# Optimization experiments

Measured on AMD Instinct MI355X. Metric: run time of the kernel, lower is better.

The kernel has to match this reference:

```python
import jax, jax.numpy as jnp
import numpy as np

B, V, J = 1024, 6890, 24
P_FEAT = (J - 1) * 9  # 207 pose-blendshape features
SMPL_PARENTS = [-1, 0, 0, 0, 1, 2, 3, 4, 5, 6, 7, 8, 9, 9, 9, 12, 13, 14, 16, 17, 18, 19, 20, 21]


def setup_inputs() -> dict:
    key = jax.random.key(0)
    ks = jax.random.split(key, 7)
    return {
        "betas": jax.random.normal(ks[0], (B, 10), jnp.float32),
        "full_pose": jax.random.normal(ks[1], (B, 72), jnp.float32) * 0.3,
        "v_template": jax.random.normal(ks[2], (1, V, 3), jnp.float32),
        "shapedirs": jax.random.normal(ks[3], (V, 3, 10), jnp.float32) * 0.01,
        "posedirs": jax.random.normal(ks[4], (P_FEAT, V * 3), jnp.float32) * 0.01,
        "J_regressor": jax.nn.softmax(jax.random.normal(ks[5], (J, V), jnp.float32), axis=-1),
        "lbs_weights": jax.nn.softmax(jax.random.normal(ks[6], (V, J), jnp.float32) * 4.0, axis=-1),
        "parents": jnp.array(SMPL_PARENTS, dtype=jnp.int32),
    }


def batch_rodrigues(rot_vecs):
    # rot_vecs: [..., 3] axis-angle -> [..., 3, 3] rotation matrices
    angle = jnp.linalg.norm(rot_vecs + 1e-8, axis=-1, keepdims=True)  # [...,1]
    axis = rot_vecs / angle
    s = jnp.sin(angle)[..., None]
    c = jnp.cos(angle)[..., None]
    kx, ky, kz = axis[..., 0], axis[..., 1], axis[..., 2]
    zeros = jnp.zeros_like(kx)
    K = jnp.stack([zeros, -kz, ky, kz, zeros, -kx, -ky, kx, zeros], axis=-1)
    K = K.reshape(rot_vecs.shape[:-1] + (3, 3))
    eye = jnp.eye(3, dtype=rot_vecs.dtype)
    return eye + s * K + (1.0 - c) * (K @ K)


def reference(betas, full_pose, v_template, shapedirs, posedirs, J_regressor, lbs_weights, parents):
    p = [int(x) for x in np.asarray(jax.device_get(parents))]  # static kinematic tree
    b = betas.shape[0]

    # 1) shape blendshapes: minimal shape
    v_shaped = v_template + jnp.einsum("bl,vkl->bvk", betas, shapedirs)  # [B,V,3]

    # 2) rest joints
    J_rest = jnp.einsum("jv,bvk->bjk", J_regressor, v_shaped)  # [B,J,3]

    # 3) pose rotations + pose blendshapes
    rot_mats = batch_rodrigues(full_pose.reshape(b, J, 3))  # [B,J,3,3]
    eye = jnp.eye(3, dtype=rot_mats.dtype)
    pose_feature = (rot_mats[:, 1:] - eye).reshape(b, P_FEAT)  # [B,207]
    v_posed = v_shaped + (pose_feature @ posedirs).reshape(b, V, 3)

    # 4) kinematic chain (sequential composition over fixed 24 joints)
    rel_joints = J_rest.at[:, 1:].add(-J_rest[:, np.array(p[1:])])  # [B,J,3]
    Tm = jnp.zeros((b, J, 4, 4), dtype=rot_mats.dtype)
    Tm = Tm.at[:, :, :3, :3].set(rot_mats)
    Tm = Tm.at[:, :, :3, 3].set(rel_joints)
    Tm = Tm.at[:, :, 3, 3].set(1.0)
    chain = [Tm[:, 0]]
    for i in range(1, J):
        chain.append(chain[p[i]] @ Tm[:, i])
    transforms = jnp.stack(chain, axis=1)  # [B,J,4,4]

    J_posed = transforms[:, :, :3, 3]  # [B,J,3]

    # relative bone transforms: subtract rotated rest joints from translation
    RJ = jnp.einsum("bjmn,bjn->bjm", transforms[:, :, :3, :3], J_rest)
    A = transforms.at[:, :, :3, 3].add(-RJ)  # [B,J,4,4]

    # 5) linear blend skinning: per-vertex weighted transform then apply
    T = jnp.einsum("vj,bjmn->bvmn", lbs_weights, A)  # [B,V,4,4]
    verts = jnp.einsum("bvmn,bvn->bvm", T[:, :, :3, :3], v_posed) + T[:, :, :3, 3]

    return verts, J_posed, J_rest, A, v_shaped
```

## Files before the change

kernel.cpp:

```cpp
#include <hip/hip_runtime.h>
#include <hip/hip_bf16.h>

#define BDIM 1024
#define VDIM 6890
#define NJ   24
#define NCOL (VDIM*3)
#define KPAD 224
#define NPAD 20736
#define NB   8
#define VPAD 6912

#define OUT_VERTS   0
#define OUT_JPOSED  21166080
#define OUT_JREST   21239808
#define OUT_A       21313536
#define OUT_VSHAPED 21706752

#define SCRF_PDT    0
#define SCRF_PF     2322432
#define SCRF_JTJS   2437120

#define WSB_PDT   0u
#define WSB_PF    9289728u
#define WSB_JTJS  9748480u
#define WSB_WHI   9752064u
#define WSB_WLO   10194432u
#define WS_NEED   10636800u

typedef __hip_bfloat16 bf16;
typedef unsigned short ushort_t;
typedef __attribute__((ext_vector_type(8))) short  short8;
typedef __attribute__((ext_vector_type(4))) float  float4v;

__device__ __forceinline__ bf16  tob(float x) { return __float2bfloat16(x); }

__device__ __forceinline__ ushort_t bf16_rne(float x) {
    unsigned u = __builtin_bit_cast(unsigned, x);
    unsigned r = (u + 0x7FFFu + ((u >> 16) & 1u)) >> 16;
    return (ushort_t)r;
}
__device__ __forceinline__ float bf16_to_f(ushort_t h) {
    unsigned u = ((unsigned)h) << 16;
    return __builtin_bit_cast(float, u);
}

__global__ __launch_bounds__(256) void k_jtjs(const float* __restrict__ jreg,
        const float* __restrict__ vt, const float* __restrict__ sd,
        float* __restrict__ jtjs) {
    int j = blockIdx.x;
    int tid = threadIdx.x;
    float acc[33];
#pragma unroll
    for (int i = 0; i < 33; i++) acc[i] = 0.f;
    for (int v = tid; v < VDIM; v += 256) {
        float r = jreg[j*VDIM + v];
#pragma unroll
        for (int m = 0; m < 3; m++) {
            acc[m] += r * vt[v*3+m];
#pragma unroll
            for (int l = 0; l < 10; l++)
                acc[3 + m*10 + l] += r * sd[(v*3+m)*10 + l];
        }
    }
    __shared__ float red[4][33];
    int lane = tid & 63, wid = tid >> 6;
#pragma unroll
    for (int i = 0; i < 33; i++) {
        float x = acc[i];
        for (int off = 32; off > 0; off >>= 1) x += __shfl_down(x, off);
        if (lane == 0) red[wid][i] = x;
    }
    __syncthreads();
    if (tid < 33)
        jtjs[j*33 + tid] = red[0][tid] + red[1][tid] + red[2][tid] + red[3][tid];
}

__global__ __launch_bounds__(256) void k_transpose(const float* __restrict__ pd,
        bf16* __restrict__ pdt) {
    __shared__ bf16 tile[32][65];
    int nt = blockIdx.x * 64;
    int kt = blockIdx.y * 32;
    int t = threadIdx.x;
    for (int i = t; i < 32*64; i += 256) {
        int kk = i >> 6, nn = i & 63;
        int k = kt + kk, n = nt + nn;
        float v = 0.f;
        if (k < 207 && n < NCOL) v = pd[k*NCOL + n];
        tile[kk][nn] = tob(v);
    }
    __syncthreads();
    for (int i = t; i < 32*64; i += 256) {
        int kk = i & 31, nn = i >> 5;
        pdt[(nt + nn)*KPAD + kt + kk] = tile[kk][nn];
    }
}

__global__ __launch_bounds__(256) void k_wpack(const float* __restrict__ lbs,
        ushort_t* __restrict__ whi, ushort_t* __restrict__ wlo) {
    int idx = blockIdx.x*256 + threadIdx.x;
    if (idx >= VPAD*32) return;
    int v = idx >> 5, j = idx & 31;
    float x = (v < VDIM && j < 24) ? lbs[v*24 + j] : 0.f;
    ushort_t h = bf16_rne(x);
    whi[idx] = h;
    wlo[idx] = bf16_rne(x - bf16_to_f(h));
}

__global__ __launch_bounds__(64) void k_pose(const float* __restrict__ betas,
        const float* __restrict__ pose, const int* __restrict__ parents,
        const float* __restrict__ jtjs, float* __restrict__ out,
        bf16* __restrict__ wspf) {
    int b = blockIdx.x, t = threadIdx.x;
    __shared__ float R[24][9];
    __shared__ float jrest[24][3];
    __shared__ float rel[24][3];
    __shared__ float ch[24][12];
    __shared__ int par[24];
    if (t < 24) {
        par[t] = parents[t];
        float rx = pose[b*72 + t*3 + 0];
        float ry = pose[b*72 + t*3 + 1];
        float rz = pose[b*72 + t*3 + 2];
        float ax = rx + 1e-8f, ay = ry + 1e-8f, az = rz + 1e-8f;
        float angle = sqrtf(ax*ax + ay*ay + az*az);
        float inv = 1.0f / angle;
        float kx = rx*inv, ky = ry*inv, kz = rz*inv;
        float s = sinf(angle), c = cosf(angle);
        float t1 = 1.0f - c;
        float q = kx*kx + ky*ky + kz*kz;
        R[t][0] = 1.f + t1*(kx*kx - q);
        R[t][1] = -s*kz + t1*kx*ky;
        R[t][2] =  s*ky + t1*kx*kz;
        R[t][3] =  s*kz + t1*kx*ky;
        R[t][4] = 1.f + t1*(ky*ky - q);
        R[t][5] = -s*kx + t1*ky*kz;
        R[t][6] = -s*ky + t1*kx*kz;
        R[t][7] =  s*kx + t1*ky*kz;
        R[t][8] = 1.f + t1*(kz*kz - q);
    }
    __syncthreads();
    for (int i = t; i < KPAD; i += 64) {
        float pf = 0.f;
        if (i < 207) {
            int j = i/9 + 1, e = i - (j-1)*9;
            pf = R[j][e] - ((e == 0 || e == 4 || e == 8) ? 1.f : 0.f);
        }
        wspf[b*KPAD + i] = tob(pf);
    }
    for (int i = t; i < 72; i += 64) {
        int j = i/3, k = i - j*3;
        const float* JJ = &jtjs[j*33];
        float s = JJ[k];
#pragma unroll
        for (int l = 0; l < 10; l++) s += JJ[3 + k*10 + l] * betas[b*10 + l];
        jrest[j][k] = s;
        out[OUT_JREST + b*72 + i] = s;
    }
    __syncthreads();
    for (int i = t; i < 72; i += 64) {
        int j = i/3, k = i - j*3;
        rel[j][k] = jrest[j][k] - (j > 0 ? jrest[par[j]][k] : 0.f);
    }
    __syncthreads();
    if (t < 12) {
        int m = t >> 2, n = t & 3;
        ch[0][t] = (n < 3) ? R[0][m*3+n] : rel[0][m];
    }
    __syncthreads();
    for (int i = 1; i < 24; i++) {
        float val = 0.f;
        if (t < 12) {
            int m = t >> 2, n = t & 3;
            int p = par[i];
            if (n < 3)
                val = ch[p][m*4+0]*R[i][n] + ch[p][m*4+1]*R[i][3+n] + ch[p][m*4+2]*R[i][6+n];
            else
                val = ch[p][m*4+0]*rel[i][0] + ch[p][m*4+1]*rel[i][1]
                    + ch[p][m*4+2]*rel[i][2] + ch[p][m*4+3];
        }
        if (t < 12) ch[i][t] = val;
        __syncthreads();
    }
    for (int i = t; i < 72; i += 64) {
        int j = i/3, k = i - j*3;
        out[OUT_JPOSED + b*72 + i] = ch[j][k*4+3];
    }
    for (int i = t; i < 384; i += 64) {
        int j = i >> 4, e = i & 15, m = e >> 2, n = e & 3;
        float v;
        if (m < 3) {
            if (n < 3) v = ch[j][m*4+n];
            else v = ch[j][m*4+3] - (ch[j][m*4+0]*jrest[j][0] + ch[j][m*4+1]*jrest[j][1]
                                   + ch[j][m*4+2]*jrest[j][2]);
        } else v = (n == 3) ? 1.f : 0.f;
        out[OUT_A + b*384 + i] = v;
    }
}

__global__ __launch_bounds__(256) void k_gemmlbs(const bf16* __restrict__ wspf,
        const bf16* __restrict__ wspdt, const float* __restrict__ betas,
        const float* __restrict__ sd, const float* __restrict__ vt,
        const ushort_t* __restrict__ whi, const ushort_t* __restrict__ wlo,
        const float* __restrict__ Amat, float* __restrict__ out) {
    __shared__ float dtile[32][196];
    const ushort_t* pf  = (const ushort_t*)wspf;
    const ushort_t* pdt = (const ushort_t*)wspdt;
    int tid  = threadIdx.x;
    int lane = tid & 63, wave = tid >> 6;
    int l15 = lane & 15, quad = lane >> 4;
    int m0 = blockIdx.y * 32;
    int v0 = blockIdx.x * 64;
    int cb = wave * 48;
    int colb = v0*3 + cb;

    {
        float4v acc[2][3] = {};
        for (int c = 0; c < 7; c++) {
            short8 a[2], bb[3];
#pragma unroll
            for (int mf = 0; mf < 2; mf++)
                a[mf] = *reinterpret_cast<const short8*>(pf + (m0 + mf*16 + l15)*KPAD + c*32 + quad*8);
#pragma unroll
            for (int nf = 0; nf < 3; nf++)
                bb[nf] = *reinterpret_cast<const short8*>(pdt + (colb + nf*16 + l15)*KPAD + c*32 + quad*8);
#pragma unroll
            for (int mf = 0; mf < 2; mf++)
#pragma unroll
                for (int nf = 0; nf < 3; nf++)
                    acc[mf][nf] = __builtin_amdgcn_mfma_f32_16x16x32_bf16(a[mf], bb[nf], acc[mf][nf], 0, 0, 0);
        }
#pragma unroll
        for (int mf = 0; mf < 2; mf++)
#pragma unroll
            for (int nf = 0; nf < 3; nf++)
#pragma unroll
                for (int r = 0; r < 4; r++)
                    dtile[mf*16 + quad*4 + r][cb + nf*16 + l15] = acc[mf][nf][r];
    }
    __syncthreads();

    int wv = __builtin_amdgcn_readfirstlane(wave);
    int v = v0 + lane;
    float* vsh = out + OUT_VSHAPED;
    if (v < VDIM) {
        float vtv[3];
#pragma unroll
        for (int m = 0; m < 3; m++) vtv[m] = vt[v*3 + m];
        float sdv[30];
#pragma unroll
        for (int i = 0; i < 30; i++) sdv[i] = sd[v*30 + i];
#pragma unroll 1
        for (int bb2 = 0; bb2 < 8; bb2++) {
            int b  = m0 + wv*8 + bb2;
            int bl = wv*8 + bb2;
            float vs[3];
#pragma unroll
            for (int m = 0; m < 3; m++) {
                float s = vtv[m];
#pragma unroll
                for (int l = 0; l < 10; l++) s += betas[b*10 + l] * sdv[m*10 + l];
                vs[m] = s;
            }
            int base = b*NCOL + v*3;
#pragma unroll
            for (int n = 0; n < 3; n++) {
                float d = dtile[bl][lane*3 + n];
                dtile[bl][lane*3 + n] = vs[n] + d;
                vsh[base + n] = vs[n];
            }
        }
    }
    __syncthreads();

    short8 bhi[4], blo[4];
#pragma unroll
    for (int nf = 0; nf < 4; nf++) {
        int vv = v0 + nf*16 + l15;
        bhi[nf] = *reinterpret_cast<const short8*>(whi + vv*32 + quad*8);
        blo[nf] = *reinterpret_cast<const short8*>(wlo + vv*32 + quad*8);
    }
    bool aval = (quad < 3) && (l15 < 12);
#pragma unroll 1
    for (int bb2 = 0; bb2 < 8; bb2++) {
        int b  = m0 + wv*8 + bb2;
        int bl = wv*8 + bb2;
        float af[8];
#pragma unroll
        for (int i = 0; i < 8; i++)
            af[i] = aval ? Amat[(size_t)b*384 + (quad*8 + i)*16 + l15] : 0.f;
        short8 ahi, alo;
#pragma unroll
        for (int i = 0; i < 8; i++) {
            ushort_t h = bf16_rne(af[i]);
            ahi[i] = (short)h;
            alo[i] = (short)bf16_rne(af[i] - bf16_to_f(h));
        }
#pragma unroll
        for (int nf = 0; nf < 4; nf++) {
            float4v acc = {};
            acc = __builtin_amdgcn_mfma_f32_16x16x32_bf16(ahi, bhi[nf], acc, 0, 0, 0);
            acc = __builtin_amdgcn_mfma_f32_16x16x32_bf16(alo, bhi[nf], acc, 0, 0, 0);
            acc = __builtin_amdgcn_mfma_f32_16x16x32_bf16(ahi, blo[nf], acc, 0, 0, 0);
            int vl = nf*16 + l15;
            float vp0 = dtile[bl][vl*3 + 0];
            float vp1 = dtile[bl][vl*3 + 1];
            float vp2 = dtile[bl][vl*3 + 2];
            if (quad < 3 && v0 + vl < VDIM) {
                float o = acc[3] + acc[0]*vp0 + acc[1]*vp1 + acc[2]*vp2;
                out[(size_t)b*NCOL + (v0 + vl)*3 + quad] = o;
            }
        }
    }
}

__global__ __launch_bounds__(256) void k_posegemm(const bf16* __restrict__ wspf,
        const bf16* __restrict__ wspdt, float* __restrict__ dout) {
    const ushort_t* pf  = (const ushort_t*)wspf;
    const ushort_t* pdt = (const ushort_t*)wspdt;
    int lane = threadIdx.x & 63;
    int wave = threadIdx.x >> 6;
    int l15 = lane & 15, quad = lane >> 4;
    int m0 = blockIdx.y * 32;
    int n0 = blockIdx.x * 256 + wave * 64;
    float4v acc[2][4] = {};
    for (int c = 0; c < 7; c++) {
        short8 a[2], bb[4];
#pragma unroll
        for (int mf = 0; mf < 2; mf++)
            a[mf] = *reinterpret_cast<const short8*>(pf + (m0 + mf*16 + l15)*KPAD + c*32 + quad*8);
#pragma unroll
        for (int nf = 0; nf < 4; nf++)
            bb[nf] = *reinterpret_cast<const short8*>(pdt + (n0 + nf*16 + l15)*KPAD + c*32 + quad*8);
#pragma unroll
        for (int mf = 0; mf < 2; mf++)
#pragma unroll
            for (int nf = 0; nf < 4; nf++)
                acc[mf][nf] = __builtin_amdgcn_mfma_f32_16x16x32_bf16(a[mf], bb[nf], acc[mf][nf], 0, 0, 0);
    }
#pragma unroll
    for (int mf = 0; mf < 2; mf++)
#pragma unroll
        for (int nf = 0; nf < 4; nf++) {
            int col = n0 + nf*16 + l15;
            if (col < NCOL) {
#pragma unroll
                for (int r = 0; r < 4; r++) {
                    int row = m0 + mf*16 + quad*4 + r;
                    dout[row*NCOL + col] = acc[mf][nf][r];
                }
            }
        }
}

__global__ __launch_bounds__(256) void k_lbs(const float* __restrict__ betas,
        const float* __restrict__ sd, const float* __restrict__ vt,
        const float* __restrict__ lbs, const float* __restrict__ Amat,
        float* __restrict__ out) {
    int tid = threadIdx.x;
    int v = blockIdx.x*256 + tid;
    if (v >= VDIM) return;
    int b0 = blockIdx.y * NB;
    float w[24];
    {
        const float4v* W4 = reinterpret_cast<const float4v*>(lbs + v*24);
#pragma unroll
        for (int q = 0; q < 6; q++) {
            float4v x = W4[q];
#pragma unroll
            for (int e = 0; e < 4; e++) w[q*4+e] = x[e];
        }
    }
    float vtv[3];
#pragma unroll
    for (int m = 0; m < 3; m++) vtv[m] = vt[v*3 + m];
    float sdv[30];
#pragma unroll
    for (int i = 0; i < 30; i++) sdv[i] = sd[v*30 + i];
    float* vsh = out + OUT_VSHAPED;
#pragma unroll 1
    for (int bb = 0; bb < NB; bb++) {
        int b = b0 + bb;
        const float* __restrict__ Ab = Amat + (size_t)b*384;
        float T[12];
#pragma unroll
        for (int e = 0; e < 12; e++) T[e] = 0.f;
#pragma unroll
        for (int j = 0; j < 24; j++) {
#pragma unroll
            for (int e = 0; e < 12; e++)
                T[e] = fmaf(w[j], Ab[j*16 + e], T[e]);
        }
        float vs[3];
#pragma unroll
        for (int m = 0; m < 3; m++) {
            float s = vtv[m];
#pragma unroll
            for (int l = 0; l < 10; l++) s += betas[b*10 + l] * sdv[m*10 + l];
            vs[m] = s;
        }
        int base = b*NCOL + v*3;
        float vp0 = vs[0] + vsh[base + 0];
        float vp1 = vs[1] + vsh[base + 1];
        float vp2 = vs[2] + vsh[base + 2];
#pragma unroll
        for (int m = 0; m < 3; m++) {
            float o = T[m*4+3] + T[m*4]*vp0 + T[m*4+1]*vp1 + T[m*4+2]*vp2;
            out[base + m] = o;
            vsh[base + m] = vs[m];
        }
    }
}

extern "C" void kernel_launch(void* const* d_in, const int* in_sizes, int n_in,
                              void* d_out, int out_size, void* d_ws, size_t ws_size,
                              hipStream_t stream) {
    const float *betas = nullptr, *pose = nullptr, *vt = nullptr, *sd = nullptr,
                *pd = nullptr, *jreg = nullptr, *lbs = nullptr;
    const int* parents = nullptr;
    for (int i = 0; i < n_in; i++) {
        switch (in_sizes[i]) {
            case 10240:   betas = (const float*)d_in[i]; break;
            case 73728:   pose  = (const float*)d_in[i]; break;
            case 20670:   vt    = (const float*)d_in[i]; break;
            case 206700:  sd    = (const float*)d_in[i]; break;
            case 4278690: pd    = (const float*)d_in[i]; break;
            case 24:      parents = (const int*)d_in[i]; break;
            case 165360:
                if (!jreg) jreg = (const float*)d_in[i];
                else       lbs  = (const float*)d_in[i];
                break;
            default: break;
        }
    }
    float* out = (float*)d_out;
    if (d_ws && ws_size >= (size_t)WS_NEED) {
        bf16*     ws_pdt  = (bf16*)((char*)d_ws + WSB_PDT);
        bf16*     ws_pf   = (bf16*)((char*)d_ws + WSB_PF);
        float*    ws_jtjs = (float*)((char*)d_ws + WSB_JTJS);
        ushort_t* ws_whi  = (ushort_t*)((char*)d_ws + WSB_WHI);
        ushort_t* ws_wlo  = (ushort_t*)((char*)d_ws + WSB_WLO);
        k_jtjs<<<24, 256, 0, stream>>>(jreg, vt, sd, ws_jtjs);
        k_transpose<<<dim3(324, 7), 256, 0, stream>>>(pd, ws_pdt);
        k_wpack<<<(VPAD*32 + 255)/256, 256, 0, stream>>>(lbs, ws_whi, ws_wlo);
        k_pose<<<BDIM, 64, 0, stream>>>(betas, pose, parents, ws_jtjs, out, ws_pf);
        k_gemmlbs<<<dim3(108, 32), 256, 0, stream>>>(ws_pf, ws_pdt, betas, sd, vt,
                                                     ws_whi, ws_wlo, out + OUT_A, out);
    } else {
        bf16*  ws_pdt  = (bf16*)(out + SCRF_PDT);
        bf16*  ws_pf   = (bf16*)(out + SCRF_PF);
        float* ws_jtjs = out + SCRF_JTJS;
        k_jtjs<<<24, 256, 0, stream>>>(jreg, vt, sd, ws_jtjs);
        k_transpose<<<dim3(324, 7), 256, 0, stream>>>(pd, ws_pdt);
        k_pose<<<BDIM, 64, 0, stream>>>(betas, pose, parents, ws_jtjs, out, ws_pf);
        k_posegemm<<<dim3(81, 32), 256, 0, stream>>>(ws_pf, ws_pdt, out + OUT_VSHAPED);
        k_lbs<<<dim3(27, BDIM/NB), 256, 0, stream>>>(betas, sd, vt, lbs, out + OUT_A, out);
    }
}
```

Baseline: 300.2 us.

## Precompute bf16 hi/lo A matrices, pad vertex tile to float4, merge prep kernels

Merges the lbs-weight packing into the joint-regressor prep kernel, removing one launch. k_pose now also writes the bone transforms as bf16 hi/lo split matrices, so the LBS stage loads ready MFMA operands instead of loading and converting fp32 per batch. The posed-vertex shared tile is stored with a 4-float stride, which allows vectorized float4 reads and writes. A __syncthreads between phases is dropped, on the reasoning that each wave only touches its own rows. The cost is extra workspace and global traffic for the A hi/lo buffers, and a larger shared-memory tile.

```diff
diff --git a/kernel.cpp b/kernel.cpp
--- a/kernel.cpp
+++ b/kernel.cpp
@@ -25,7 +25,9 @@
 #define WSB_JTJS  9748480u
 #define WSB_WHI   9752064u
 #define WSB_WLO   10194432u
-#define WS_NEED   10636800u
+#define WSB_AHI   10636800u
+#define WSB_ALO   11685376u
+#define WS_NEED   12733952u
 
 typedef __hip_bfloat16 bf16;
 typedef unsigned short ushort_t;
@@ -44,9 +46,21 @@
     return __builtin_bit_cast(float, u);
 }
 
-__global__ __launch_bounds__(256) void k_jtjs(const float* __restrict__ jreg,
+__global__ __launch_bounds__(256) void k_prep(const float* __restrict__ jreg,
         const float* __restrict__ vt, const float* __restrict__ sd,
-        float* __restrict__ jtjs) {
+        const float* __restrict__ lbs, float* __restrict__ jtjs,
+        ushort_t* __restrict__ whi, ushort_t* __restrict__ wlo) {
+    if (blockIdx.x >= 24) {
+        if (!whi) return;
+        int idx = (blockIdx.x - 24)*256 + threadIdx.x;
+        if (idx >= VPAD*32) return;
+        int v = idx >> 5, j = idx & 31;
+        float x = (v < VDIM && j < 24) ? lbs[v*24 + j] : 0.f;
+        ushort_t h = bf16_rne(x);
+        whi[idx] = h;
+        wlo[idx] = bf16_rne(x - bf16_to_f(h));
+        return;
+    }
     int j = blockIdx.x;
     int tid = threadIdx.x;
     float acc[33];
@@ -95,21 +109,11 @@
     }
 }
 
-__global__ __launch_bounds__(256) void k_wpack(const float* __restrict__ lbs,
-        ushort_t* __restrict__ whi, ushort_t* __restrict__ wlo) {
-    int idx = blockIdx.x*256 + threadIdx.x;
-    if (idx >= VPAD*32) return;
-    int v = idx >> 5, j = idx & 31;
-    float x = (v < VDIM && j < 24) ? lbs[v*24 + j] : 0.f;
-    ushort_t h = bf16_rne(x);
-    whi[idx] = h;
-    wlo[idx] = bf16_rne(x - bf16_to_f(h));
-}
-
 __global__ __launch_bounds__(64) void k_pose(const float* __restrict__ betas,
         const float* __restrict__ pose, const int* __restrict__ parents,
         const float* __restrict__ jtjs, float* __restrict__ out,
-        bf16* __restrict__ wspf) {
+        bf16* __restrict__ wspf, ushort_t* __restrict__ ahi,
+        ushort_t* __restrict__ alo) {
     int b = blockIdx.x, t = threadIdx.x;
     __shared__ float R[24][9];
     __shared__ float jrest[24][3];
@@ -195,14 +199,30 @@
         } else v = (n == 3) ? 1.f : 0.f;
         out[OUT_A + b*384 + i] = v;
     }
+    if (ahi) {
+        for (int i = t; i < 512; i += 64) {
+            int e = i >> 5, j = i & 31;
+            float v = 0.f;
+            if (j < 24 && e < 12) {
+                int m = e >> 2, n = e & 3;
+                if (n < 3) v = ch[j][m*4+n];
+                else v = ch[j][m*4+3] - (ch[j][m*4+0]*jrest[j][0] + ch[j][m*4+1]*jrest[j][1]
+                                       + ch[j][m*4+2]*jrest[j][2]);
+            }
+            ushort_t h = bf16_rne(v);
+            ahi[b*512 + i] = h;
+            alo[b*512 + i] = bf16_rne(v - bf16_to_f(h));
+        }
+    }
 }
 
 __global__ __launch_bounds__(256) void k_gemmlbs(const bf16* __restrict__ wspf,
         const bf16* __restrict__ wspdt, const float* __restrict__ betas,
         const float* __restrict__ sd, const float* __restrict__ vt,
         const ushort_t* __restrict__ whi, const ushort_t* __restrict__ wlo,
-        const float* __restrict__ Amat, float* __restrict__ out) {
-    __shared__ float dtile[32][196];
+        const ushort_t* __restrict__ ahi, const ushort_t* __restrict__ alo,
+        float* __restrict__ out) {
+    __shared__ float dtile[32][260];
     const ushort_t* pf  = (const ushort_t*)wspf;
     const ushort_t* pdt = (const ushort_t*)wspdt;
     int tid  = threadIdx.x;
@@ -230,12 +250,16 @@
                     acc[mf][nf] = __builtin_amdgcn_mfma_f32_16x16x32_bf16(a[mf], bb[nf], acc[mf][nf], 0, 0, 0);
         }
 #pragma unroll
-        for (int mf = 0; mf < 2; mf++)
-#pragma unroll
-            for (int nf = 0; nf < 3; nf++)
+        for (int nf = 0; nf < 3; nf++) {
+            int c0 = cb + nf*16 + l15;
+            int vv = c0 / 3, rr = c0 - vv*3;
+            int ad = vv*4 + rr;
+#pragma unroll
+            for (int mf = 0; mf < 2; mf++)
 #pragma unroll
                 for (int r = 0; r < 4; r++)
-                    dtile[mf*16 + quad*4 + r][cb + nf*16 + l15] = acc[mf][nf][r];
+                    dtile[mf*16 + quad*4 + r][ad] = acc[mf][nf][r];
+        }
     }
     __syncthreads();
 
@@ -249,7 +273,7 @@
         float sdv[30];
 #pragma unroll
         for (int i = 0; i < 30; i++) sdv[i] = sd[v*30 + i];
-#pragma unroll 1
+#pragma unroll 2
         for (int bb2 = 0; bb2 < 8; bb2++) {
             int b  = m0 + wv*8 + bb2;
             int bl = wv*8 + bb2;
@@ -261,16 +285,17 @@
                 for (int l = 0; l < 10; l++) s += betas[b*10 + l] * sdv[m*10 + l];
                 vs[m] = s;
             }
+            float4v* slot = reinterpret_cast<float4v*>(&dtile[bl][lane*4]);
+            float4v d = *slot;
+            float4v vp;
+            vp[0] = vs[0] + d[0]; vp[1] = vs[1] + d[1];
+            vp[2] = vs[2] + d[2]; vp[3] = 0.f;
+            *slot = vp;
             int base = b*NCOL + v*3;
 #pragma unroll
-            for (int n = 0; n < 3; n++) {
-                float d = dtile[bl][lane*3 + n];
-                dtile[bl][lane*3 + n] = vs[n] + d;
-                vsh[base + n] = vs[n];
-            }
-        }
-    }
-    __syncthreads();
+            for (int n = 0; n < 3; n++) vsh[base + n] = vs[n];
+        }
+    }
 
     short8 bhi[4], blo[4];
 #pragma unroll
@@ -279,35 +304,33 @@
         bhi[nf] = *reinterpret_cast<const short8*>(whi + vv*32 + quad*8);
         blo[nf] = *reinterpret_cast<const short8*>(wlo + vv*32 + quad*8);
     }
-    bool aval = (quad < 3) && (l15 < 12);
+    const ushort_t* ah = ahi + (size_t)(m0 + wv*8)*512 + l15*32 + quad*8;
+    const ushort_t* al = alo + (size_t)(m0 + wv*8)*512 + l15*32 + quad*8;
 #pragma unroll 1
-    for (int bb2 = 0; bb2 < 8; bb2++) {
-        int b  = m0 + wv*8 + bb2;
-        int bl = wv*8 + bb2;
-        float af[8];
-#pragma unroll
-        for (int i = 0; i < 8; i++)
-            af[i] = aval ? Amat[(size_t)b*384 + (quad*8 + i)*16 + l15] : 0.f;
-        short8 ahi, alo;
-#pragma unroll
-        for (int i = 0; i < 8; i++) {
-            ushort_t h = bf16_rne(af[i]);
-            ahi[i] = (short)h;
-            alo[i] = (short)bf16_rne(af[i] - bf16_to_f(h));
-        }
-#pragma unroll
-        for (int nf = 0; nf < 4; nf++) {
-            float4v acc = {};
-            acc = __builtin_amdgcn_mfma_f32_16x16x32_bf16(ahi, bhi[nf], acc, 0, 0, 0);
-            acc = __builtin_amdgcn_mfma_f32_16x16x32_bf16(alo, bhi[nf], acc, 0, 0, 0);
-            acc = __builtin_amdgcn_mfma_f32_16x16x32_bf16(ahi, blo[nf], acc, 0, 0, 0);
-            int vl = nf*16 + l15;
-            float vp0 = dtile[bl][vl*3 + 0];
-            float vp1 = dtile[bl][vl*3 + 1];
-            float vp2 = dtile[bl][vl*3 + 2];
-            if (quad < 3 && v0 + vl < VDIM) {
-                float o = acc[3] + acc[0]*vp0 + acc[1]*vp1 + acc[2]*vp2;
-                out[(size_t)b*NCOL + (v0 + vl)*3 + quad] = o;
+    for (int g = 0; g < 2; g++) {
+        short8 a_hi[4], a_lo[4];
+#pragma unroll
+        for (int k = 0; k < 4; k++) {
+            a_hi[k] = *reinterpret_cast<const short8*>(ah + (size_t)(g*4 + k)*512);
+            a_lo[k] = *reinterpret_cast<const short8*>(al + (size_t)(g*4 + k)*512);
+        }
+#pragma unroll
+        for (int k = 0; k < 4; k++) {
+            int bb2 = g*4 + k;
+            int b  = m0 + wv*8 + bb2;
+            int bl = wv*8 + bb2;
+#pragma unroll
+            for (int nf = 0; nf < 4; nf++) {
+                float4v acc = {};
+                acc = __builtin_amdgcn_mfma_f32_16x16x32_bf16(a_hi[k], bhi[nf], acc, 0, 0, 0);
+                acc = __builtin_amdgcn_mfma_f32_16x16x32_bf16(a_lo[k], bhi[nf], acc, 0, 0, 0);
+                acc = __builtin_amdgcn_mfma_f32_16x16x32_bf16(a_hi[k], blo[nf], acc, 0, 0, 0);
+                int vl = nf*16 + l15;
+                float4v vp = *reinterpret_cast<const float4v*>(&dtile[bl][vl*4]);
+                if (quad < 3 && v0 + vl < VDIM) {
+                    float o = acc[3] + acc[0]*vp[0] + acc[1]*vp[1] + acc[2]*vp[2];
+                    out[(size_t)b*NCOL + (size_t)(v0 + vl)*3 + quad] = o;
+                }
             }
         }
     }
@@ -439,19 +462,22 @@
         float*    ws_jtjs = (float*)((char*)d_ws + WSB_JTJS);
         ushort_t* ws_whi  = (ushort_t*)((char*)d_ws + WSB_WHI);
         ushort_t* ws_wlo  = (ushort_t*)((char*)d_ws + WSB_WLO);
-        k_jtjs<<<24, 256, 0, stream>>>(jreg, vt, sd, ws_jtjs);
+        ushort_t* ws_ahi  = (ushort_t*)((char*)d_ws + WSB_AHI);
+        ushort_t* ws_alo  = (ushort_t*)((char*)d_ws + WSB_ALO);
+        k_prep<<<888, 256, 0, stream>>>(jreg, vt, sd, lbs, ws_jtjs, ws_whi, ws_wlo);
         k_transpose<<<dim3(324, 7), 256, 0, stream>>>(pd, ws_pdt);
-        k_wpack<<<(VPAD*32 + 255)/256, 256, 0, stream>>>(lbs, ws_whi, ws_wlo);
-        k_pose<<<BDIM, 64, 0, stream>>>(betas, pose, parents, ws_jtjs, out, ws_pf);
+        k_pose<<<BDIM, 64, 0, stream>>>(betas, pose, parents, ws_jtjs, out, ws_pf,
+                                        ws_ahi, ws_alo);
         k_gemmlbs<<<dim3(108, 32), 256, 0, stream>>>(ws_pf, ws_pdt, betas, sd, vt,
-                                                     ws_whi, ws_wlo, out + OUT_A, out);
+                                                     ws_whi, ws_wlo, ws_ahi, ws_alo, out);
     } else {
         bf16*  ws_pdt  = (bf16*)(out + SCRF_PDT);
         bf16*  ws_pf   = (bf16*)(out + SCRF_PF);
         float* ws_jtjs = out + SCRF_JTJS;
-        k_jtjs<<<24, 256, 0, stream>>>(jreg, vt, sd, ws_jtjs);
+        k_prep<<<24, 256, 0, stream>>>(jreg, vt, sd, lbs, ws_jtjs, nullptr, nullptr);
         k_transpose<<<dim3(324, 7), 256, 0, stream>>>(pd, ws_pdt);
-        k_pose<<<BDIM, 64, 0, stream>>>(betas, pose, parents, ws_jtjs, out, ws_pf);
+        k_pose<<<BDIM, 64, 0, stream>>>(betas, pose, parents, ws_jtjs, out, ws_pf,
+                                        nullptr, nullptr);
         k_posegemm<<<dim3(81, 32), 256, 0, stream>>>(ws_pf, ws_pdt, out + OUT_VSHAPED);
         k_lbs<<<dim3(27, BDIM/NB), 256, 0, stream>>>(betas, sd, vt, lbs, out + OUT_A, out);
     }
```

Result: no change. 304.0 us (+1.3%).
